# Kernel tuning notes

Measured on AMD Instinct MI355X. Metric: run time of the kernel, lower is better.

## Reference

```python
import jax, jax.numpy as jnp
import numpy as np

KEY_SIZE = 256
EPS = 1e-8  # torch F.cosine_similarity default eps


def setup_inputs() -> dict:
    key = jax.random.key(0)
    k1, k2 = jax.random.split(key)
    B, M, K, V = 2048, 100000, KEY_SIZE, 256
    query = jax.random.normal(k1, (B, K), dtype=jnp.float32)
    memory = jax.random.normal(k2, (M, K + V), dtype=jnp.float32)
    return {"query": query, "memory": memory}


def reference(query, memory):
    # memory: [M, K+V] -> keys [M, K], values [M, V]
    keys = memory[:, :KEY_SIZE]
    values = memory[:, KEY_SIZE:]
    # cosine similarity: (q . k) / max(|q|*|k|, eps)  -> [B, M]
    dots = jnp.einsum('bk,mk->bm', query, keys)
    qn = jnp.linalg.norm(query, axis=1)  # [B]
    kn = jnp.linalg.norm(keys, axis=1)   # [M]
    sims = dots / jnp.maximum(qn[:, None] * kn[None, :], EPS)
    # top-1 over memory dim, then gather values -> [B, V]
    idx = jnp.argmax(sims, axis=1)
    return values[idx]
```

## Files before the change

kernel.cpp:

```cpp
#include <hip/hip_runtime.h>
#include <hip/hip_fp16.h>
#include <float.h>

#define MKEY 256
#define NMEM 100000
#define NPAD 100096
#define NQ   2048
#define BM 128
#define BN 128
#define NTILES 782
#define BLKPAD 800
#define GRID (128 * 98)
#define KB16 (NPAD / 16)
#define QS (127.0f / 6.0f)
#define SS2 ((6.0f / 127.0f) * (6.0f / 127.0f))
#define GDELTA 0.04f
#define GINVD  25.0f

typedef int i32x4 __attribute__((ext_vector_type(4)));

__device__ inline void gll16(const void* g, void* l) {
  __builtin_amdgcn_global_load_lds(
      (const __attribute__((address_space(1))) unsigned*)g,
      (__attribute__((address_space(3))) unsigned*)l, 16, 0, 0);
}

__device__ inline int pack_i8x4(float4 v) {
  int c0 = max(-127, min(127, __float2int_rn(v.x * QS)));
  int c1 = max(-127, min(127, __float2int_rn(v.y * QS)));
  int c2 = max(-127, min(127, __float2int_rn(v.z * QS)));
  int c3 = max(-127, min(127, __float2int_rn(v.w * QS)));
  return (c0 & 255) | ((c1 & 255) << 8) | ((c2 & 255) << 16) | ((c3 & 255) << 24);
}

__device__ inline int dot4i8(int a, int b, int s) {
#if __has_builtin(__builtin_amdgcn_sdot4)
  return __builtin_amdgcn_sdot4(a, b, s, false);
#else
#pragma unroll
  for (int k = 0; k < 4; ++k) {
    const int av = (a << (24 - 8 * k)) >> 24;
    const int bv = (b << (24 - 8 * k)) >> 24;
    s += av * bv;
  }
  return s;
#endif
}

__device__ inline float rowmax16(float x) {
  int y;
  y = __builtin_amdgcn_update_dpp(0, __float_as_int(x), 0x121, 0xF, 0xF, true);
  x = fmaxf(x, __int_as_float(y));
  y = __builtin_amdgcn_update_dpp(0, __float_as_int(x), 0x122, 0xF, 0xF, true);
  x = fmaxf(x, __int_as_float(y));
  y = __builtin_amdgcn_update_dpp(0, __float_as_int(x), 0x124, 0xF, 0xF, true);
  x = fmaxf(x, __int_as_float(y));
  y = __builtin_amdgcn_update_dpp(0, __float_as_int(x), 0x128, 0xF, 0xF, true);
  return fmaxf(x, __int_as_float(y));
}

__global__ void convert(const float* __restrict__ q, const float* __restrict__ mem,
                        int* __restrict__ qi, int* __restrict__ ki,
                        float* __restrict__ rkn) {
  const int b = blockIdx.x, t = threadIdx.x;
  if (b >= KB16) {
    const int i = (b - KB16) * 256 + t;
    const float4 v = *(const float4*)&q[(size_t)i * 4];
    qi[i] = pack_i8x4(v);
    return;
  }
  const int row = b * 16 + (t >> 4);
  const int c = t & 15;
  if (row < NMEM) {
    const float* src = &mem[(size_t)row * 512 + c * 16];
    const float4 v0 = *(const float4*)&src[0];
    const float4 v1 = *(const float4*)&src[4];
    const float4 v2 = *(const float4*)&src[8];
    const float4 v3 = *(const float4*)&src[12];
    float ss = v0.x * v0.x + v0.y * v0.y + v0.z * v0.z + v0.w * v0.w +
               v1.x * v1.x + v1.y * v1.y + v1.z * v1.z + v1.w * v1.w +
               v2.x * v2.x + v2.y * v2.y + v2.z * v2.z + v2.w * v2.w +
               v3.x * v3.x + v3.y * v3.y + v3.z * v3.z + v3.w * v3.w;
#pragma unroll
    for (int off = 8; off >= 1; off >>= 1) ss += __shfl_xor(ss, off, 64);
    int4 pk;
    pk.x = pack_i8x4(v0); pk.y = pack_i8x4(v1);
    pk.z = pack_i8x4(v2); pk.w = pack_i8x4(v3);
    *(int4*)&ki[(size_t)row * 64 + c * 4] = pk;
    if (c == 0) rkn[row] = 1.0f / sqrtf(fmaxf(ss, 1e-30f));
  } else {
    *(int4*)&ki[(size_t)row * 64 + c * 4] = make_int4(0, 0, 0, 0);
    if (c == 0) rkn[row] = 0.f;
  }
}

__global__ __launch_bounds__(256, 4) void gemm_screen(
    const int* __restrict__ qi, const int* __restrict__ ki,
    const float* __restrict__ rkn,
    unsigned long long* __restrict__ bcode8, float* __restrict__ bmaxB) {
  __shared__ __align__(128) char smem[32768];

  const int id = blockIdx.x;
  const int mtile = (id >> 3) & 15;
  const int ntile = (id & 7) + 8 * (id >> 7);
  if (ntile >= NTILES) return;

  const int t = threadIdx.x;
  const int w = t >> 6;
  const int lane = t & 63;
  const int wr = w >> 1, wc = w & 1;
  const int q16 = lane >> 4, l16 = lane & 15;

  const int swz64 = ((lane & 3) ^ ((lane >> 2) & 3)) * 16;
  int soff4[4];
#pragma unroll
  for (int c = 0; c < 4; ++c)
    soff4[c] = ((w & 1) * 64 + c * 16 + (lane >> 2)) * 256 + swz64;
  const char* const asrc = (const char*)((w < 2) ? qi : ki) +
                           (size_t)(((w < 2) ? mtile : ntile) * 128) * 256;
  char* const dbase = smem + ((w < 2) ? 0 : 16384) + (w & 1) * 4096;

#define STG(p, s)                                         \
  do {                                                    \
    const char* _s = asrc + (s) * 64;                     \
    char* _d = dbase + (p) * 8192;                        \
    _Pragma("unroll")                                     \
    for (int c = 0; c < 4; ++c)                           \
      gll16(_s + soff4[c], _d + c * 1024);                \
  } while (0)

  i32x4 acc[4][4];
#pragma unroll
  for (int i = 0; i < 4; i++)
#pragma unroll
    for (int j = 0; j < 4; j++) acc[i][j] = (i32x4){0, 0, 0, 0};

  const int pc4 = (q16 ^ (l16 & 3)) * 16;

  STG(0, 0);
  __syncthreads();
#pragma unroll
  for (int s = 0; s < 4; ++s) {
    if (s < 3) STG((s + 1) & 1, s + 1);
    const int p = (s & 1) * 8192;
    i32x4 av[4], bv[4];
#pragma unroll
    for (int i = 0; i < 4; i++)
      av[i] = *(const i32x4*)&smem[p + (64 * wr + 16 * i + l16) * 64 + pc4];
#pragma unroll
    for (int j = 0; j < 4; j++)
      bv[j] = *(const i32x4*)&smem[16384 + p + (64 * wc + 16 * j + l16) * 64 + pc4];
#pragma unroll
    for (int i = 0; i < 4; i++)
#pragma unroll
      for (int j = 0; j < 4; j++)
        acc[i][j] = __builtin_amdgcn_mfma_i32_16x16x64_i8(av[i], bv[j], acc[i][j], 0, 0, 0);
    __syncthreads();
  }
#undef STG

  float rk[4];
#pragma unroll
  for (int j = 0; j < 4; j++) {
    const int ncol = ntile * BN + 64 * wc + 16 * j + l16;
    rk[j] = (ncol < NMEM) ? rkn[ncol] * SS2 : 0.f;
  }
  float (*cg)[132] = (float(*)[132])smem;
#pragma unroll
  for (int i = 0; i < 4; ++i)
#pragma unroll
    for (int j = 0; j < 4; ++j)
#pragma unroll
      for (int r = 0; r < 4; ++r) {
        const float m = rowmax16((float)acc[i][j][r] * rk[j]);
        if (l16 == 0)
          cg[wc * 4 + j][64 * wr + 16 * i + 4 * q16 + r] = m;
      }
  __syncthreads();
  if (t < 128) {
    float v[8];
#pragma unroll
    for (int g = 0; g < 8; ++g) v[g] = cg[g][t];
    float bm = fmaxf(fmaxf(fmaxf(v[0], v[1]), fmaxf(v[2], v[3])),
                     fmaxf(fmaxf(v[4], v[5]), fmaxf(v[6], v[7])));
    bmaxB[(size_t)ntile * NQ + mtile * 128 + t] = bm;
    unsigned long long cw = 0;
#pragma unroll
    for (int g = 0; g < 8; ++g) {
      int code = (int)((bm - v[g]) * GINVD);
      code = min(255, max(0, code));
      cw |= (unsigned long long)(unsigned)code << (8 * g);
    }
    bcode8[(size_t)ntile * NQ + mtile * 128 + t] = cw;
  }
}

__global__ __launch_bounds__(256) void transpose_blk(const float* __restrict__ in,
                                                     float* __restrict__ outp) {
  __shared__ float tl[32][33];
  const int bid = blockIdx.x;
  const int ntt = bid % 25, qt = bid / 25;
  const int r0 = ntt * 32, c0 = qt * 32;
  const int tx = threadIdx.x & 31, ty = threadIdx.x >> 5;
#pragma unroll
  for (int k = 0; k < 4; ++k) {
    const int r = r0 + ty + 8 * k;
    tl[ty + 8 * k][tx] = (r < NTILES) ? in[(size_t)r * NQ + c0 + tx] : -FLT_MAX;
  }
  __syncthreads();
#pragma unroll
  for (int k = 0; k < 4; ++k) {
    const int qq = c0 + ty + 8 * k;
    const int nt = r0 + tx;
    if (nt < NTILES) outp[(size_t)qq * BLKPAD + nt] = tl[tx][ty + 8 * k];
  }
}

__global__ __launch_bounds__(256) void rescore_gather(
    const float* __restrict__ q, const float* __restrict__ mem,
    const int* __restrict__ qi8, const int* __restrict__ ki8,
    const float* __restrict__ rkn, const float* __restrict__ bmaxQ,
    const unsigned long long* __restrict__ bcode8, float* __restrict__ out) {
  __shared__ float red2[4];
  __shared__ int blist[64];
  __shared__ int nblk;
  __shared__ int glist[128];
  __shared__ int ng;
  __shared__ int rlist[256];
  __shared__ int nrow;
  __shared__ double wb[4];
  __shared__ int wbi[4];
  __shared__ int widx;

  const int qid = blockIdx.x;
  const int t = threadIdx.x, w = t >> 6, lane = t & 63;

  const float4 qv = *(const float4*)&q[(size_t)qid * 256 + lane * 4];
  float ss = qv.x * qv.x + qv.y * qv.y + qv.z * qv.z + qv.w * qv.w;
#pragma unroll
  for (int off = 32; off >= 1; off >>= 1) ss += __shfl_xor(ss, off, 64);
  const float qn = sqrtf(ss);
  const float margin = 1.8e-2f * qn;

  int4 qreg[4];
#pragma unroll
  for (int k = 0; k < 4; ++k)
    qreg[k] = *(const int4*)&qi8[(size_t)qid * 64 + (lane & 3) * 16 + k * 4];

  if (t == 0) { nblk = 0; ng = 0; nrow = 0; }
  const float* bq = &bmaxQ[(size_t)qid * BLKPAD];

  float gm = -FLT_MAX;
  for (int i = t; i < NTILES; i += 256) gm = fmaxf(gm, bq[i]);
#pragma unroll
  for (int off = 32; off >= 1; off >>= 1) gm = fmaxf(gm, __shfl_xor(gm, off, 64));
  if (lane == 0) red2[w] = gm;
  __syncthreads();
  gm = fmaxf(fmaxf(red2[0], red2[1]), fmaxf(red2[2], red2[3]));
  const float thresh = gm - margin;

  for (int i = t; i < NTILES; i += 256)
    if (bq[i] >= thresh) {
      int p = atomicAdd(&nblk, 1);
      if (p < 64) blist[p] = i;
    }
  __syncthreads();
  const int nb_ = min(nblk, 64);

  for (int idx = t; idx < nb_ * 8; idx += 256) {
    const int nt = blist[idx >> 3], gl = idx & 7;
    const unsigned long long cw = bcode8[(size_t)nt * NQ + qid];
    const int code = (int)((cw >> (8 * gl)) & 255);
    if ((float)code * GDELTA <= bq[nt] - thresh + 1e-6f) {
      int p = atomicAdd(&ng, 1);
      if (p < 128) glist[p] = nt * 8 + gl;
    }
  }
  __syncthreads();
  const int ng_ = min(ng, 128);

  for (int c = w; c < ng_; c += 4) {
    const int row = glist[c] * 16 + (lane >> 2);
    int idot = 0;
#pragma unroll
    for (int k = 0; k < 4; ++k) {
      const int4 kv = *(const int4*)&ki8[(size_t)row * 64 + (lane & 3) * 16 + k * 4];
      idot = dot4i8(kv.x, qreg[k].x, idot);
      idot = dot4i8(kv.y, qreg[k].y, idot);
      idot = dot4i8(kv.z, qreg[k].z, idot);
      idot = dot4i8(kv.w, qreg[k].w, idot);
    }
    idot += __shfl_xor(idot, 1, 64);
    idot += __shfl_xor(idot, 2, 64);
    if ((lane & 3) == 0 && row < NMEM) {
      const float sh = (float)idot * (rkn[row] * SS2);
      if (sh >= thresh) {
        int p = atomicAdd(&nrow, 1);
        if (p < 256) rlist[p] = row;
      }
    }
  }
  __syncthreads();
  const int nr = min(nrow, 256);

  double bestv = -1e300;
  int bestidx = 0x7fffffff;
  for (int c = w; c < nr; c += 4) {
    const int row = rlist[c];
    const float4 kv = *(const float4*)&mem[(size_t)row * 512 + lane * 4];
    double d = (double)kv.x * qv.x + (double)kv.y * qv.y +
               (double)kv.z * qv.z + (double)kv.w * qv.w;
    double s2 = (double)kv.x * kv.x + (double)kv.y * kv.y +
                (double)kv.z * kv.z + (double)kv.w * kv.w;
#pragma unroll
    for (int off = 32; off >= 1; off >>= 1) {
      d += __shfl_xor(d, off, 64);
      s2 += __shfl_xor(s2, off, 64);
    }
    if (lane == 0) {
      const double score = d / sqrt(s2 > 1e-300 ? s2 : 1e-300);
      if (score > bestv || (score == bestv && row < bestidx)) {
        bestv = score;
        bestidx = row;
      }
    }
  }
  if (lane == 0) { wb[w] = bestv; wbi[w] = bestidx; }
  __syncthreads();
  if (t == 0) {
    double bv = wb[0];
    int bi = wbi[0];
#pragma unroll
    for (int w2 = 1; w2 < 4; ++w2)
      if (wb[w2] > bv || (wb[w2] == bv && wbi[w2] < bi)) {
        bv = wb[w2];
        bi = wbi[w2];
      }
    widx = bi;
  }
  __syncthreads();
  out[(size_t)qid * 256 + t] = mem[(size_t)widx * 512 + 256 + t];
}

extern "C" void kernel_launch(void* const* d_in, const int* in_sizes, int n_in,
                              void* d_out, int out_size, void* d_ws, size_t ws_size,
                              hipStream_t stream) {
  const float* query = (const float*)d_in[0];
  const float* memory = (const float*)d_in[1];
  float* out = (float*)d_out;

  char* p = (char*)d_ws;
  int* qi = (int*)p; p += (size_t)NQ * 64 * 4;
  int* ki = (int*)p; p += (size_t)NPAD * 64 * 4;
  float* rkn = (float*)p; p += (size_t)NPAD * 4;
  float* bmaxB = (float*)p; p += (size_t)NTILES * NQ * 4;
  float* bmaxQ = (float*)p; p += (size_t)NQ * BLKPAD * 4;
  unsigned long long* bcode8 = (unsigned long long*)p;
  p += (size_t)NTILES * NQ * 8;

  hipLaunchKernelGGL(convert, dim3(KB16 + NQ * MKEY / 1024), dim3(256), 0, stream,
                     query, memory, qi, ki, rkn);
  hipLaunchKernelGGL(gemm_screen, dim3(GRID), dim3(256), 0, stream,
                     qi, ki, rkn, bcode8, bmaxB);
  hipLaunchKernelGGL(transpose_blk, dim3(25 * 64), dim3(256), 0, stream, bmaxB, bmaxQ);
  hipLaunchKernelGGL(rescore_gather, dim3(NQ), dim3(256), 0, stream,
                     query, memory, qi, ki, rkn, bmaxQ, bcode8, out);
}
```

Before: 388.9 us.

## Swap MFMA operand roles so per-group max reduces within registers

Swaps the A and B operands of the int8 MFMA so that memory keys map to the accumulator's register and row dimension and queries map to lanes. The per-16-key group max can then be taken over the 4 accumulator registers plus two cross-row shuffles, replacing the 16-lane DPP reduction done for every register. It also changes the LDS swizzle and read pattern to cut bank conflicts, and drops the padded LDS staging layout. The epilogue loads 16 key norms per thread instead of 4, and correctness depends on the new swizzle and the read offsets matching each other.

Result: faster. 373.9 us (-3.9%).

```diff
diff --git a/kernel.cpp b/kernel.cpp
--- a/kernel.cpp
+++ b/kernel.cpp
@@ -47,18 +47,6 @@
 #endif
 }
 
-__device__ inline float rowmax16(float x) {
-  int y;
-  y = __builtin_amdgcn_update_dpp(0, __float_as_int(x), 0x121, 0xF, 0xF, true);
-  x = fmaxf(x, __int_as_float(y));
-  y = __builtin_amdgcn_update_dpp(0, __float_as_int(x), 0x122, 0xF, 0xF, true);
-  x = fmaxf(x, __int_as_float(y));
-  y = __builtin_amdgcn_update_dpp(0, __float_as_int(x), 0x124, 0xF, 0xF, true);
-  x = fmaxf(x, __int_as_float(y));
-  y = __builtin_amdgcn_update_dpp(0, __float_as_int(x), 0x128, 0xF, 0xF, true);
-  return fmaxf(x, __int_as_float(y));
-}
-
 __global__ void convert(const float* __restrict__ q, const float* __restrict__ mem,
                         int* __restrict__ qi, int* __restrict__ ki,
                         float* __restrict__ rkn) {
@@ -111,7 +99,7 @@
   const int wr = w >> 1, wc = w & 1;
   const int q16 = lane >> 4, l16 = lane & 15;
 
-  const int swz64 = ((lane & 3) ^ ((lane >> 2) & 3)) * 16;
+  const int swz64 = ((lane & 3) ^ ((lane >> 3) & 3)) * 16;
   int soff4[4];
 #pragma unroll
   for (int c = 0; c < 4; ++c)
@@ -135,7 +123,7 @@
 #pragma unroll
     for (int j = 0; j < 4; j++) acc[i][j] = (i32x4){0, 0, 0, 0};
 
-  const int pc4 = (q16 ^ (l16 & 3)) * 16;
+  const int pc4 = (q16 ^ ((l16 >> 1) & 3)) * 16;
 
   STG(0, 0);
   __syncthreads();
@@ -146,10 +134,10 @@
     i32x4 av[4], bv[4];
 #pragma unroll
     for (int i = 0; i < 4; i++)
-      av[i] = *(const i32x4*)&smem[p + (64 * wr + 16 * i + l16) * 64 + pc4];
+      av[i] = *(const i32x4*)&smem[16384 + p + (64 * wr + 16 * i + l16) * 64 + pc4];
 #pragma unroll
     for (int j = 0; j < 4; j++)
-      bv[j] = *(const i32x4*)&smem[16384 + p + (64 * wc + 16 * j + l16) * 64 + pc4];
+      bv[j] = *(const i32x4*)&smem[p + (64 * wc + 16 * j + l16) * 64 + pc4];
 #pragma unroll
     for (int i = 0; i < 4; i++)
 #pragma unroll
@@ -159,30 +147,36 @@
   }
 #undef STG
 
-  float rk[4];
-#pragma unroll
-  for (int j = 0; j < 4; j++) {
-    const int ncol = ntile * BN + 64 * wc + 16 * j + l16;
-    rk[j] = (ncol < NMEM) ? rkn[ncol] * SS2 : 0.f;
-  }
-  float (*cg)[132] = (float(*)[132])smem;
+  float rkv[4][4];
 #pragma unroll
   for (int i = 0; i < 4; ++i)
 #pragma unroll
-    for (int j = 0; j < 4; ++j)
-#pragma unroll
-      for (int r = 0; r < 4; ++r) {
-        const float m = rowmax16((float)acc[i][j][r] * rk[j]);
-        if (l16 == 0)
-          cg[wc * 4 + j][64 * wr + 16 * i + 4 * q16 + r] = m;
-      }
+    for (int r = 0; r < 4; ++r) {
+      const int ncol = ntile * BN + 64 * wr + 16 * i + 4 * q16 + r;
+      rkv[i][r] = (ncol < NMEM) ? rkn[ncol] * SS2 : 0.f;
+    }
+  float (*cg)[128] = (float(*)[128])smem;
+#pragma unroll
+  for (int i = 0; i < 4; ++i) {
+#pragma unroll
+    for (int j = 0; j < 4; ++j) {
+      float m = fmaxf(fmaxf((float)acc[i][j][0] * rkv[i][0],
+                            (float)acc[i][j][1] * rkv[i][1]),
+                      fmaxf((float)acc[i][j][2] * rkv[i][2],
+                            (float)acc[i][j][3] * rkv[i][3]));
+      m = fmaxf(m, __shfl_xor(m, 16, 64));
+      m = fmaxf(m, __shfl_xor(m, 32, 64));
+      if (q16 == 0)
+        cg[4 * wr + i][64 * wc + 16 * j + l16] = m;
+    }
+  }
   __syncthreads();
   if (t < 128) {
     float v[8];
 #pragma unroll
     for (int g = 0; g < 8; ++g) v[g] = cg[g][t];
-    float bm = fmaxf(fmaxf(fmaxf(v[0], v[1]), fmaxf(v[2], v[3])),
-                     fmaxf(fmaxf(v[4], v[5]), fmaxf(v[6], v[7])));
+    const float bm = fmaxf(fmaxf(fmaxf(v[0], v[1]), fmaxf(v[2], v[3])),
+                           fmaxf(fmaxf(v[4], v[5]), fmaxf(v[6], v[7])));
     bmaxB[(size_t)ntile * NQ + mtile * 128 + t] = bm;
     unsigned long long cw = 0;
 #pragma unroll
```
